# Performance work log

Measured on AMD Instinct MI355X. Metric: run time of the kernel, lower is better.

Reference implementation:

```python
import jax, jax.numpy as jnp
import numpy as np

EPS = 1e-8  # torch F.cosine_similarity default eps
NEG = -1e9  # masked_fill value


def setup_inputs() -> dict:
    key = jax.random.key(0)
    k1, k2, k3 = jax.random.split(key, 3)
    B, Sq, Sk, D = 4, 2048, 2048, 1024
    query = jax.random.normal(k1, (B, Sq, 1, D), dtype=jnp.float32)
    key_t = jax.random.normal(k2, (B, 1, Sk, D), dtype=jnp.float32)
    mask = jax.random.randint(k3, (B, Sk), 0, 2, dtype=jnp.int32)
    return {"query": query, "key": key_t, "mask": mask}


def reference(query, key, mask):
    # query: [B, Sq, 1, D], key: [B, 1, Sk, D]
    q = query[:, :, 0, :]  # [B, Sq, D]
    k = key[:, 0, :, :]    # [B, Sk, D]
    # cosine_similarity(q, k, dim=3) = (q.k) / (max(|q|,eps) * max(|k|,eps))
    qn = jnp.maximum(jnp.linalg.norm(q, axis=-1), EPS)  # [B, Sq]
    kn = jnp.maximum(jnp.linalg.norm(k, axis=-1), EPS)  # [B, Sk]
    dot = jnp.einsum('bqd,bkd->bqk', q, k)              # [B, Sq, Sk]
    scores = dot / (qn[:, :, None] * kn[:, None, :])
    # mask.unsqueeze(1).repeat(1, Sq, 1) -> broadcast [B, 1, Sk] over Sq
    scores = jnp.where(mask[:, None, :] == 0, NEG, scores)
    return scores
```

## Files before the change

### kernel.cpp

```cpp
#include <hip/hip_runtime.h>
#include <hip/hip_bf16.h>
#include <stdint.h>


constexpr int B_  = 4;
constexpr int SQ  = 2048;
constexpr int SK  = 2048;
constexpr int D_  = 1024;
constexpr int BM  = 128;
constexpr int BN  = 128;
constexpr int BK  = 32;

typedef __attribute__((ext_vector_type(8))) short    short8;
typedef __attribute__((ext_vector_type(4))) float    f32x4;
typedef __attribute__((ext_vector_type(4))) unsigned uint4v;
typedef unsigned int u32;

__device__ inline unsigned pack_bf16(float lo, float hi) {
  union { float f; unsigned u; } a, b;
  a.f = lo; b.f = hi;
  return __builtin_amdgcn_perm(b.u, a.u, 0x07060302u);
}

__device__ inline void async_ld16(const void* g, void* l) {
  __builtin_amdgcn_global_load_lds((const __attribute__((address_space(1))) u32*)g,
                                   (__attribute__((address_space(3))) u32*)l, 16, 0, 0);
}

constexpr int ROWS_Q = B_ * SQ;
constexpr int ROWS_T = B_ * (SQ + SK);

__global__ __launch_bounds__(256) void convert_norm(
    const float* __restrict__ Q, const float* __restrict__ Km,
    unsigned short* __restrict__ Qb, unsigned short* __restrict__ Kb,
    float* __restrict__ invQ, float* __restrict__ invK)
{
  const int row  = blockIdx.x * 4 + (threadIdx.x >> 6);
  const int lane = threadIdx.x & 63;

  const float* src; unsigned short* dst; float* inv;
  if (row < ROWS_Q) {
    src = Q  + (size_t)row * D_;
    dst = Qb + (size_t)row * D_;
    inv = invQ + row;
  } else {
    int r = row - ROWS_Q;
    src = Km + (size_t)r * D_;
    dst = Kb + (size_t)r * D_;
    inv = invK + r;
  }

  const f32x4* s4 = (const f32x4*)(src + lane * 16);
  f32x4 v[4];
  #pragma unroll
  for (int i = 0; i < 4; ++i) v[i] = s4[i];

  float ss = 0.0f;
  unsigned p[8];
  #pragma unroll
  for (int i = 0; i < 4; ++i) {
    p[2*i]   = pack_bf16(v[i].x, v[i].y);
    p[2*i+1] = pack_bf16(v[i].z, v[i].w);
    ss += v[i].x*v[i].x + v[i].y*v[i].y + v[i].z*v[i].z + v[i].w*v[i].w;
  }
  uint4v w0 = {p[0], p[1], p[2], p[3]};
  uint4v w1 = {p[4], p[5], p[6], p[7]};
  uint4v* d4 = (uint4v*)(dst + lane * 16);
  d4[0] = w0; d4[1] = w1;

  #pragma unroll
  for (int off = 32; off > 0; off >>= 1) ss += __shfl_xor(ss, off);
  if (lane == 0) *inv = 1.0f / fmaxf(sqrtf(ss), 1e-8f);
}

__global__ __launch_bounds__(256, 2) void ca_gemm_bf(
    const unsigned short* __restrict__ Qb,
    const unsigned short* __restrict__ Kb,
    const float* __restrict__ invQ,
    const float* __restrict__ invK,
    const int*   __restrict__ mask,
    float*       __restrict__ out)
{
  __shared__ __align__(16) unsigned short As[BM * BK];
  __shared__ __align__(16) unsigned short Bs[BN * BK];

  const int tid  = threadIdx.x;
  const int lane = tid & 63;
  const int w    = tid >> 6;
  const int b    = blockIdx.z;
  const int tm0  = blockIdx.y * BM;
  const int tn0  = blockIdx.x * BN;

  const int srow = lane >> 2;
  const int soff = (lane & 3) * 16;

  const char* qrow = (const char*)(Qb + ((size_t)b * SQ + tm0 + w * 32 + srow) * D_) + soff;
  const char* krow = (const char*)(Kb + ((size_t)b * SK + tn0 + w * 32 + srow) * D_) + soff;
  const size_t rstep16 = (size_t)16 * D_ * 2;

  unsigned short* ldsA0 = &As[(w * 32 +  0) * BK];
  unsigned short* ldsA1 = &As[(w * 32 + 16) * BK];
  unsigned short* ldsB0 = &Bs[(w * 32 +  0) * BK];
  unsigned short* ldsB1 = &Bs[(w * 32 + 16) * BK];

  f32x4 zero4 = {0.0f, 0.0f, 0.0f, 0.0f};
  f32x4 acc[4][4];
  #pragma unroll
  for (int i = 0; i < 4; ++i)
    #pragma unroll
    for (int j = 0; j < 4; ++j) acc[i][j] = zero4;

  const int wm = (w >> 1) * 64;
  const int wn = (w & 1) * 64;
  const int lr = lane & 15;
  const int lq = lane >> 4;

  for (int k0 = 0; k0 < D_; k0 += BK) {
    __syncthreads();
    const size_t kb = (size_t)k0 * 2;
    async_ld16(qrow + kb,           ldsA0);
    async_ld16(qrow + kb + rstep16, ldsA1);
    async_ld16(krow + kb,           ldsB0);
    async_ld16(krow + kb + rstep16, ldsB1);
    __syncthreads();

    short8 af[4], bf[4];
    #pragma unroll
    for (int t = 0; t < 4; ++t)
      af[t] = *(const short8*)&As[(wm + t * 16 + lr) * BK + lq * 8];
    #pragma unroll
    for (int t = 0; t < 4; ++t)
      bf[t] = *(const short8*)&Bs[(wn + t * 16 + lr) * BK + lq * 8];

    #pragma unroll
    for (int i = 0; i < 4; ++i)
      #pragma unroll
      for (int j = 0; j < 4; ++j)
        acc[i][j] = __builtin_amdgcn_mfma_f32_16x16x32_bf16(af[i], bf[j], acc[i][j], 0, 0, 0);
  }

  #pragma unroll
  for (int tn = 0; tn < 4; ++tn) {
    const int gc = tn0 + wn + tn * 16 + lr;
    const int mk = mask[b * SK + gc];
    const float ib = invK[b * SK + gc];
    #pragma unroll
    for (int tm = 0; tm < 4; ++tm) {
      const int lrow = wm + tm * 16 + lq * 4;
      #pragma unroll
      for (int r = 0; r < 4; ++r) {
        const float ia = invQ[b * SQ + tm0 + lrow + r];
        float v = mk ? acc[tm][tn][r] * ia * ib : -1000000000.0f;
        out[((size_t)b * SQ + tm0 + lrow + r) * SK + gc] = v;
      }
    }
  }
}

constexpr int LDK = 40;

__global__ __launch_bounds__(256, 2) void ca_gemm(
    const float* __restrict__ Q, const float* __restrict__ Km,
    const int* __restrict__ mask, float* __restrict__ out)
{
  __shared__ __align__(16) short As[BM * LDK];
  __shared__ __align__(16) short Bs[BN * LDK];
  __shared__ float ssA_part[256];
  __shared__ float ssB_part[256];
  __shared__ float invA[BM];
  __shared__ float invB[BN];

  const int tid  = threadIdx.x;
  const int lane = tid & 63;
  const int w    = tid >> 6;
  const int b    = blockIdx.z;
  const int tm0  = blockIdx.y * BM;
  const int tn0  = blockIdx.x * BN;

  const int ra = tid >> 1;
  const int ka = (tid & 1) * 16;

  const float* qp = Q  + ((size_t)b * SQ + tm0 + ra) * D_ + ka;
  const float* kp = Km + ((size_t)b * SK + tn0 + ra) * D_ + ka;

  f32x4 zero4 = {0.0f, 0.0f, 0.0f, 0.0f};
  f32x4 acc[4][4];
  #pragma unroll
  for (int i = 0; i < 4; ++i)
    #pragma unroll
    for (int j = 0; j < 4; ++j) acc[i][j] = zero4;

  float ssA = 0.0f, ssB = 0.0f;

  const int wm = (w >> 1) * 64;
  const int wn = (w & 1) * 64;
  const int lr = lane & 15;
  const int lq = lane >> 4;

  short* aw = &As[ra * LDK + ka];
  short* bw = &Bs[ra * LDK + ka];

  for (int k0 = 0; k0 < D_; k0 += BK) {
    f32x4 av[4], bv[4];
    #pragma unroll
    for (int i = 0; i < 4; ++i) av[i] = *(const f32x4*)(qp + 4 * i);
    #pragma unroll
    for (int i = 0; i < 4; ++i) bv[i] = *(const f32x4*)(kp + 4 * i);
    qp += BK; kp += BK;

    unsigned pa[8], pb[8];
    #pragma unroll
    for (int i = 0; i < 4; ++i) {
      pa[2*i]   = pack_bf16(av[i].x, av[i].y);
      pa[2*i+1] = pack_bf16(av[i].z, av[i].w);
      pb[2*i]   = pack_bf16(bv[i].x, bv[i].y);
      pb[2*i+1] = pack_bf16(bv[i].z, bv[i].w);
      ssA += av[i].x*av[i].x + av[i].y*av[i].y + av[i].z*av[i].z + av[i].w*av[i].w;
      ssB += bv[i].x*bv[i].x + bv[i].y*bv[i].y + bv[i].z*bv[i].z + bv[i].w*bv[i].w;
    }

    __syncthreads();
    {
      uint4v wa0 = {pa[0], pa[1], pa[2], pa[3]};
      uint4v wa1 = {pa[4], pa[5], pa[6], pa[7]};
      uint4v wb0 = {pb[0], pb[1], pb[2], pb[3]};
      uint4v wb1 = {pb[4], pb[5], pb[6], pb[7]};
      *(uint4v*)(aw)     = wa0;
      *(uint4v*)(aw + 8) = wa1;
      *(uint4v*)(bw)     = wb0;
      *(uint4v*)(bw + 8) = wb1;
    }
    __syncthreads();

    short8 af[4], bf[4];
    #pragma unroll
    for (int t = 0; t < 4; ++t)
      af[t] = *(const short8*)&As[(wm + t * 16 + lr) * LDK + lq * 8];
    #pragma unroll
    for (int t = 0; t < 4; ++t)
      bf[t] = *(const short8*)&Bs[(wn + t * 16 + lr) * LDK + lq * 8];

    #pragma unroll
    for (int i = 0; i < 4; ++i)
      #pragma unroll
      for (int j = 0; j < 4; ++j)
        acc[i][j] = __builtin_amdgcn_mfma_f32_16x16x32_bf16(af[i], bf[j], acc[i][j], 0, 0, 0);
  }

  ssA_part[tid] = ssA;
  ssB_part[tid] = ssB;
  __syncthreads();
  if (tid < BM) {
    float s = ssA_part[2 * tid] + ssA_part[2 * tid + 1];
    invA[tid] = 1.0f / fmaxf(sqrtf(s), 1e-8f);
  } else {
    int r = tid - BM;
    float s = ssB_part[2 * r] + ssB_part[2 * r + 1];
    invB[r] = 1.0f / fmaxf(sqrtf(s), 1e-8f);
  }
  __syncthreads();

  #pragma unroll
  for (int tn = 0; tn < 4; ++tn) {
    const int lc = wn + tn * 16 + lr;
    const int gc = tn0 + lc;
    const int mk = mask[b * SK + gc];
    const float ib = invB[lc];
    #pragma unroll
    for (int tm = 0; tm < 4; ++tm) {
      const int lrow = wm + tm * 16 + lq * 4;
      #pragma unroll
      for (int r = 0; r < 4; ++r) {
        float v = mk ? acc[tm][tn][r] * invA[lrow + r] * ib : -1000000000.0f;
        out[((size_t)b * SQ + tm0 + lrow + r) * SK + gc] = v;
      }
    }
  }
}

extern "C" void kernel_launch(void* const* d_in, const int* in_sizes, int n_in,
                              void* d_out, int out_size, void* d_ws, size_t ws_size,
                              hipStream_t stream) {
  const float* Q    = (const float*)d_in[0];
  const float* Km   = (const float*)d_in[1];
  const int*   mask = (const int*)d_in[2];
  float*       out  = (float*)d_out;

  const size_t nQ   = (size_t)B_ * SQ * D_;
  const size_t nK   = (size_t)B_ * SK * D_;
  const size_t need = (nQ + nK) * 2
                    + (size_t)B_ * (SQ + SK) * 4;
  if (ws_size >= need) {
    unsigned short* Qb  = (unsigned short*)d_ws;
    unsigned short* Kb  = Qb + nQ;
    float*          iQ  = (float*)(Kb + nK);
    float*          iK  = iQ + (size_t)B_ * SQ;
    convert_norm<<<ROWS_T / 4, 256, 0, stream>>>(Q, Km, Qb, Kb, iQ, iK);
    dim3 grid(SK / BN, SQ / BM, B_);
    ca_gemm_bf<<<grid, dim3(256), 0, stream>>>(Qb, Kb, iQ, iK, mask, out);
  } else {
    dim3 grid(SK / BN, SQ / BM, B_);
    ca_gemm<<<grid, dim3(256), 0, stream>>>(Q, Km, mask, out);
  }
}
```

Baseline: 167.2 us.

## Switch GEMM path from bf16 to fp8 MFMA with swizzled LDS tiles

Converts Q and K to fp8 (e4m3) instead of bf16 during the normalization pass and replaces the 16x16x32 bf16 MFMA with the 16x16x128 scaled f8f6f4 MFMA, using a 128-byte K tile per iteration. LDS is filled with XOR-swizzled 16-byte chunks to avoid bank conflicts on the wider fragment reads. This halves input staging bytes and increases math throughput per instruction. The cost is substantially reduced precision of the dot product, since fp8 has only a 3-bit mantissa, and cosine scores may drift beyond the tolerance.

```diff
diff --git a/kernel.cpp b/kernel.cpp
--- a/kernel.cpp
+++ b/kernel.cpp
@@ -9,10 +9,13 @@
 constexpr int D_  = 1024;
 constexpr int BM  = 128;
 constexpr int BN  = 128;
+constexpr int BKF = 128;
 constexpr int BK  = 32;
 
 typedef __attribute__((ext_vector_type(8))) short    short8;
 typedef __attribute__((ext_vector_type(4))) float    f32x4;
+typedef __attribute__((ext_vector_type(4))) int      int4v;
+typedef __attribute__((ext_vector_type(8))) int      int8v;
 typedef __attribute__((ext_vector_type(4))) unsigned uint4v;
 typedef unsigned int u32;
 
@@ -30,15 +33,15 @@
 constexpr int ROWS_Q = B_ * SQ;
 constexpr int ROWS_T = B_ * (SQ + SK);
 
-__global__ __launch_bounds__(256) void convert_norm(
+__global__ __launch_bounds__(256) void convert_fp8(
     const float* __restrict__ Q, const float* __restrict__ Km,
-    unsigned short* __restrict__ Qb, unsigned short* __restrict__ Kb,
+    uint8_t* __restrict__ Qb, uint8_t* __restrict__ Kb,
     float* __restrict__ invQ, float* __restrict__ invK)
 {
   const int row  = blockIdx.x * 4 + (threadIdx.x >> 6);
   const int lane = threadIdx.x & 63;
 
-  const float* src; unsigned short* dst; float* inv;
+  const float* src; uint8_t* dst; float* inv;
   if (row < ROWS_Q) {
     src = Q  + (size_t)row * D_;
     dst = Qb + (size_t)row * D_;
@@ -56,33 +59,32 @@
   for (int i = 0; i < 4; ++i) v[i] = s4[i];
 
   float ss = 0.0f;
-  unsigned p[8];
+  unsigned p[4];
   #pragma unroll
   for (int i = 0; i < 4; ++i) {
-    p[2*i]   = pack_bf16(v[i].x, v[i].y);
-    p[2*i+1] = pack_bf16(v[i].z, v[i].w);
+    unsigned d = (unsigned)__builtin_amdgcn_cvt_pk_fp8_f32(v[i].x, v[i].y, 0, false);
+    d = (unsigned)__builtin_amdgcn_cvt_pk_fp8_f32(v[i].z, v[i].w, (int)d, true);
+    p[i] = d;
     ss += v[i].x*v[i].x + v[i].y*v[i].y + v[i].z*v[i].z + v[i].w*v[i].w;
   }
   uint4v w0 = {p[0], p[1], p[2], p[3]};
-  uint4v w1 = {p[4], p[5], p[6], p[7]};
-  uint4v* d4 = (uint4v*)(dst + lane * 16);
-  d4[0] = w0; d4[1] = w1;
+  *(uint4v*)(dst + lane * 16) = w0;
 
   #pragma unroll
   for (int off = 32; off > 0; off >>= 1) ss += __shfl_xor(ss, off);
   if (lane == 0) *inv = 1.0f / fmaxf(sqrtf(ss), 1e-8f);
 }
 
-__global__ __launch_bounds__(256, 2) void ca_gemm_bf(
-    const unsigned short* __restrict__ Qb,
-    const unsigned short* __restrict__ Kb,
+__global__ __launch_bounds__(256, 2) void ca_gemm_fp8(
+    const uint8_t* __restrict__ Qb,
+    const uint8_t* __restrict__ Kb,
     const float* __restrict__ invQ,
     const float* __restrict__ invK,
     const int*   __restrict__ mask,
     float*       __restrict__ out)
 {
-  __shared__ __align__(16) unsigned short As[BM * BK];
-  __shared__ __align__(16) unsigned short Bs[BN * BK];
+  __shared__ __align__(16) uint8_t As[BM * BKF];
+  __shared__ __align__(16) uint8_t Bs[BN * BKF];
 
   const int tid  = threadIdx.x;
   const int lane = tid & 63;
@@ -91,17 +93,15 @@
   const int tm0  = blockIdx.y * BM;
   const int tn0  = blockIdx.x * BN;
 
-  const int srow = lane >> 2;
-  const int soff = (lane & 3) * 16;
-
-  const char* qrow = (const char*)(Qb + ((size_t)b * SQ + tm0 + w * 32 + srow) * D_) + soff;
-  const char* krow = (const char*)(Kb + ((size_t)b * SK + tn0 + w * 32 + srow) * D_) + soff;
-  const size_t rstep16 = (size_t)16 * D_ * 2;
-
-  unsigned short* ldsA0 = &As[(w * 32 +  0) * BK];
-  unsigned short* ldsA1 = &As[(w * 32 + 16) * BK];
-  unsigned short* ldsB0 = &Bs[(w * 32 +  0) * BK];
-  unsigned short* ldsB1 = &Bs[(w * 32 + 16) * BK];
+  const int srow   = lane >> 3;
+  const int gchunk = (lane & 7) ^ srow;
+
+  const uint8_t* qrow = Qb + ((size_t)b * SQ + tm0 + w * 32 + srow) * D_ + gchunk * 16;
+  const uint8_t* krow = Kb + ((size_t)b * SK + tn0 + w * 32 + srow) * D_ + gchunk * 16;
+  const size_t rstep8 = (size_t)8 * D_;
+
+  uint8_t* ldsA = As + (size_t)(w * 32) * BKF;
+  uint8_t* ldsB = Bs + (size_t)(w * 32) * BKF;
 
   f32x4 zero4 = {0.0f, 0.0f, 0.0f, 0.0f};
   f32x4 acc[4][4];
@@ -115,28 +115,42 @@
   const int lr = lane & 15;
   const int lq = lane >> 4;
 
-  for (int k0 = 0; k0 < D_; k0 += BK) {
+  for (int k0 = 0; k0 < D_; k0 += BKF) {
     __syncthreads();
-    const size_t kb = (size_t)k0 * 2;
-    async_ld16(qrow + kb,           ldsA0);
-    async_ld16(qrow + kb + rstep16, ldsA1);
-    async_ld16(krow + kb,           ldsB0);
-    async_ld16(krow + kb + rstep16, ldsB1);
+    #pragma unroll
+    for (int i = 0; i < 4; ++i)
+      async_ld16(qrow + k0 + i * rstep8, ldsA + i * 8 * BKF);
+    #pragma unroll
+    for (int i = 0; i < 4; ++i)
+      async_ld16(krow + k0 + i * rstep8, ldsB + i * 8 * BKF);
     __syncthreads();
 
-    short8 af[4], bf[4];
-    #pragma unroll
-    for (int t = 0; t < 4; ++t)
-      af[t] = *(const short8*)&As[(wm + t * 16 + lr) * BK + lq * 8];
-    #pragma unroll
-    for (int t = 0; t < 4; ++t)
-      bf[t] = *(const short8*)&Bs[(wn + t * 16 + lr) * BK + lq * 8];
+    int8v af[4], bf[4];
+    #pragma unroll
+    for (int t = 0; t < 4; ++t) {
+      const int r  = wm + t * 16 + lr;
+      const int sw = r & 7;
+      const int4v* rp = (const int4v*)(As + (size_t)r * BKF);
+      int4v lo = rp[(2 * lq) ^ sw];
+      int4v hi = rp[(2 * lq + 1) ^ sw];
+      af[t] = (int8v){lo.x, lo.y, lo.z, lo.w, hi.x, hi.y, hi.z, hi.w};
+    }
+    #pragma unroll
+    for (int t = 0; t < 4; ++t) {
+      const int r  = wn + t * 16 + lr;
+      const int sw = r & 7;
+      const int4v* rp = (const int4v*)(Bs + (size_t)r * BKF);
+      int4v lo = rp[(2 * lq) ^ sw];
+      int4v hi = rp[(2 * lq + 1) ^ sw];
+      bf[t] = (int8v){lo.x, lo.y, lo.z, lo.w, hi.x, hi.y, hi.z, hi.w};
+    }
 
     #pragma unroll
     for (int i = 0; i < 4; ++i)
       #pragma unroll
       for (int j = 0; j < 4; ++j)
-        acc[i][j] = __builtin_amdgcn_mfma_f32_16x16x32_bf16(af[i], bf[j], acc[i][j], 0, 0, 0);
+        acc[i][j] = __builtin_amdgcn_mfma_scale_f32_16x16x128_f8f6f4(
+            af[i], bf[j], acc[i][j], 0, 0, 0, 127, 0, 127);
   }
 
   #pragma unroll
@@ -288,16 +302,15 @@
 
   const size_t nQ   = (size_t)B_ * SQ * D_;
   const size_t nK   = (size_t)B_ * SK * D_;
-  const size_t need = (nQ + nK) * 2
-                    + (size_t)B_ * (SQ + SK) * 4;
+  const size_t need = nQ + nK + (size_t)B_ * (SQ + SK) * 4;
   if (ws_size >= need) {
-    unsigned short* Qb  = (unsigned short*)d_ws;
-    unsigned short* Kb  = Qb + nQ;
-    float*          iQ  = (float*)(Kb + nK);
-    float*          iK  = iQ + (size_t)B_ * SQ;
-    convert_norm<<<ROWS_T / 4, 256, 0, stream>>>(Q, Km, Qb, Kb, iQ, iK);
+    uint8_t* Qb = (uint8_t*)d_ws;
+    uint8_t* Kb = Qb + nQ;
+    float*   iQ = (float*)(Kb + nK);
+    float*   iK = iQ + (size_t)B_ * SQ;
+    convert_fp8<<<ROWS_T / 4, 256, 0, stream>>>(Q, Km, Qb, Kb, iQ, iK);
     dim3 grid(SK / BN, SQ / BM, B_);
-    ca_gemm_bf<<<grid, dim3(256), 0, stream>>>(Qb, Kb, iQ, iK, mask, out);
+    ca_gemm_fp8<<<grid, dim3(256), 0, stream>>>(Qb, Kb, iQ, iK, mask, out);
   } else {
     dim3 grid(SK / BN, SQ / BM, B_);
     ca_gemm<<<grid, dim3(256), 0, stream>>>(Q, Km, mask, out);
```

Measured after the change: 312.9 us. 1.87x slower.
